# Optimization experiments

Measured on AMD Instinct MI355X. Metric: run time of the kernel, lower is better.

Reference implementation:

```python
import jax, jax.numpy as jnp
import numpy as np

N_NODES = 100000
N_EDGES = 3200000
D = 64
NUM_RELS = 20
HID_ATTR = 32
OUT_ATTR = 10


def setup_inputs() -> dict:
    key = jax.random.key(0)
    ks = jax.random.split(key, 10)
    h = jax.random.normal(ks[0], (N_NODES, D), dtype=jnp.float32)
    src = jax.random.randint(ks[1], (N_EDGES,), 0, N_NODES)
    dst = jax.random.randint(ks[2], (N_EDGES,), 0, N_NODES)
    etype = jax.random.randint(ks[3], (N_EDGES,), 0, NUM_RELS)
    # RGCN relation weights (num_bases == num_rels, so no basis decomposition)
    s1 = (2.0 / (D + D)) ** 0.5 * (2.0 ** 0.5)  # xavier w/ relu gain, approx
    W1 = jax.random.normal(ks[4], (NUM_RELS, D, D), dtype=jnp.float32) * s1
    W2 = jax.random.normal(ks[5], (NUM_RELS, D, D), dtype=jnp.float32) * s1
    # Attributor MLP params (torch Linear: y = x @ W.T + b; stored here as [in,out])
    A1_w = jax.random.normal(ks[6], (D, HID_ATTR), dtype=jnp.float32) * (1.0 / D ** 0.5)
    A1_b = jnp.zeros((HID_ATTR,), dtype=jnp.float32)
    A2_w = jax.random.normal(ks[7], (HID_ATTR, OUT_ATTR), dtype=jnp.float32) * (1.0 / HID_ATTR ** 0.5)
    A2_b = jnp.zeros((OUT_ATTR,), dtype=jnp.float32)
    return {"h": h, "src": src, "dst": dst, "etype": etype,
            "W1": W1, "W2": W2, "A1_w": A1_w, "A1_b": A1_b,
            "A2_w": A2_w, "A2_b": A2_b}


def _rgcn_layer(h, W, src, dst, etype, activation):
    # Transform all nodes by every relation once (avoids [E,d,d] weight gather),
    # then gather the relation-specific transformed source feature per edge.
    n = h.shape[0]
    t = jnp.einsum('nd,rdo->rno', h, W)          # [R, N, d_out]
    msg = t[etype, src]                           # [E, d_out] irregular gather
    agg = jax.ops.segment_sum(msg, dst, num_segments=n)  # scatter-sum to nodes
    return activation(agg) if activation is not None else agg


def reference(h, src, dst, etype, W1, W2, A1_w, A1_b, A2_w, A2_b):
    # hidden RGCN layer (relu), output RGCN layer (no activation, no bias)
    h1 = _rgcn_layer(h, W1, src, dst, etype, jax.nn.relu)
    h2 = _rgcn_layer(h1, W2, src, dst, etype, None)
    # mean_nodes over the single graph -> [1, D]; Attributor MLP (dropout in eval = identity)
    g = jnp.mean(h2, axis=0, keepdims=True)
    a = jax.nn.relu(g @ A1_w + A1_b)
    a = jax.nn.sigmoid(a @ A2_w + A2_b)
    return (h2, a)
```

## Files before the change

kernel.cpp:

```cpp
#include <hip/hip_runtime.h>
#include <hip/hip_bf16.h>
#include <math.h>
#include <stdint.h>

#define N_NODES 100000
#define N_EDGES 3200000
#define D 64
#define NUM_RELS 20
#define HID_ATTR 32
#define OUT_ATTR 10
#define PADR 72

#define BUCKET_DSTS 256
#define NB 391
#define PA_THREADS 512
#define PA_EPT 16
#define PA_CHUNK (PA_THREADS * PA_EPT)
#define PA_GRID 391
#define PB_BINS (BUCKET_DSTS * NUM_RELS)
#define REL_HALF 10

typedef __attribute__((ext_vector_type(8))) short bf16x8;
typedef __attribute__((ext_vector_type(4))) float f32x4;

static __device__ __forceinline__ unsigned short f2bf(float x) {
    unsigned u = __builtin_bit_cast(unsigned, x);
    unsigned r = (u + 0x7FFFu + ((u >> 16) & 1u)) >> 16;
    return (unsigned short)r;
}
static __device__ __forceinline__ float bf2f(unsigned short b) {
    return __builtin_bit_cast(float, (unsigned)b << 16);
}
static __device__ __forceinline__ float bf2f_lo(unsigned u) {
    return __builtin_bit_cast(float, u << 16);
}
static __device__ __forceinline__ float bf2f_hi(unsigned u) {
    return __builtin_bit_cast(float, u & 0xFFFF0000u);
}
static __device__ __forceinline__ unsigned cvt_pk_bf16(float lo, float hi) {
    unsigned r;
    asm("v_cvt_pk_bf16_f32 %0, %1, %2" : "=v"(r) : "v"(lo), "v"(hi));
    return r;
}


__global__ void hist_bucket_kernel(const int* __restrict__ dst, int* __restrict__ hist) {
    __shared__ int h[NB];
    for (int i = threadIdx.x; i < NB; i += PA_THREADS) h[i] = 0;
    __syncthreads();
    int base = blockIdx.x * PA_CHUNK;
#pragma unroll
    for (int k = 0; k < PA_EPT; ++k) {
        int e = base + k * PA_THREADS + threadIdx.x;
        if (e < N_EDGES) atomicAdd(&h[dst[e] >> 8], 1);
    }
    __syncthreads();
    for (int i = threadIdx.x; i < NB; i += PA_THREADS)
        if (h[i]) atomicAdd(&hist[i], h[i]);
}

__global__ void scan_bucket_kernel(const int* __restrict__ hist, int* __restrict__ bbase,
                                   int* __restrict__ bcur, int* __restrict__ off_node) {
    __shared__ int s[512];
    int t = threadIdx.x;
    int v = (t < NB) ? hist[t] : 0;
    s[t] = v;
    __syncthreads();
    for (int d2 = 1; d2 < 512; d2 <<= 1) {
        int x = (t >= d2) ? s[t - d2] : 0;
        __syncthreads();
        s[t] += x;
        __syncthreads();
    }
    if (t < NB) {
        int b = s[t] - v;
        bbase[t] = b;
        bcur[t] = b;
    }
    if (t == 0) {
        bbase[NB] = N_EDGES;
        off_node[N_NODES] = N_EDGES;
    }
}

__global__ __launch_bounds__(PA_THREADS) void passA_kernel(
    const int* __restrict__ src, const int* __restrict__ dst,
    const int* __restrict__ etype, int* __restrict__ bcur,
    unsigned* __restrict__ tmp) {
    __shared__ int h[NB];
    __shared__ int gb[NB];
    __shared__ int c[NB];
    for (int i = threadIdx.x; i < NB; i += PA_THREADS) h[i] = 0;
    __syncthreads();
    int base = blockIdx.x * PA_CHUNK;
    int d[PA_EPT];
#pragma unroll
    for (int k = 0; k < PA_EPT; ++k) {
        int e = base + k * PA_THREADS + threadIdx.x;
        d[k] = (e < N_EDGES) ? dst[e] : -1;
        if (d[k] >= 0) atomicAdd(&h[d[k] >> 8], 1);
    }
    __syncthreads();
    for (int i = threadIdx.x; i < NB; i += PA_THREADS) {
        int n = h[i];
        gb[i] = n ? atomicAdd(&bcur[i], n) : 0;
        c[i] = 0;
    }
    __syncthreads();
#pragma unroll
    for (int k = 0; k < PA_EPT; ++k) {
        int e = base + k * PA_THREADS + threadIdx.x;
        if (d[k] >= 0) {
            int b = d[k] >> 8;
            int sv = src[e], r = etype[e];
            int pos = gb[b] + atomicAdd(&c[b], 1);
            tmp[pos] = ((unsigned)(d[k] & 255) << 22) | ((unsigned)sv << 5) | (unsigned)r;
        }
    }
}

__global__ __launch_bounds__(512) void passB_kernel(
    const unsigned* __restrict__ tmp, const int* __restrict__ bbase,
    int* __restrict__ edgedata, int* __restrict__ off_node,
    int* __restrict__ off_half) {
    __shared__ int binpos[PB_BINS];
    __shared__ int ssum[512];
    int t = threadIdx.x;
    int b = blockIdx.x;
    int beg = bbase[b], end = bbase[b + 1];
    for (int i = t; i < PB_BINS; i += 512) binpos[i] = 0;
    __syncthreads();
    for (int i = beg + t; i < end; i += 512) {
        unsigned v = tmp[i];
        int key = (int)(v >> 22) * NUM_RELS + (int)(v & 31u);
        atomicAdd(&binpos[key], 1);
    }
    __syncthreads();
    int loc[10];
    int sum = 0;
#pragma unroll
    for (int j = 0; j < 10; ++j) {
        loc[j] = sum;
        sum += binpos[t * 10 + j];
    }
    ssum[t] = sum;
    __syncthreads();
    for (int d2 = 1; d2 < 512; d2 <<= 1) {
        int x = (t >= d2) ? ssum[t - d2] : 0;
        __syncthreads();
        ssum[t] += x;
        __syncthreads();
    }
    int tbase = beg + ((t > 0) ? ssum[t - 1] : 0);
#pragma unroll
    for (int j = 0; j < 10; ++j) binpos[t * 10 + j] = tbase + loc[j];
    __syncthreads();
    for (int dl = t; dl < BUCKET_DSTS; dl += 512) {
        off_node[b * BUCKET_DSTS + dl] = binpos[dl * NUM_RELS];
        off_half[b * BUCKET_DSTS + dl] = binpos[dl * NUM_RELS + REL_HALF];
    }
    __syncthreads();
    for (int i = beg + t; i < end; i += 512) {
        unsigned v = tmp[i];
        int key = (int)(v >> 22) * NUM_RELS + (int)(v & 31u);
        int pos = atomicAdd(&binpos[key], 1);
        edgedata[pos] = (int)(((v >> 5) & 0x1FFFFu) | ((v & 31u) << 17));
    }
}


__global__ void f2b_kernel(const float* __restrict__ in, unsigned short* __restrict__ out,
                           int n4) {
    int i = blockIdx.x * 256 + threadIdx.x;
    if (i >= n4) return;
    float4 v = ((const float4*)in)[i];
    ushort4 o;
    o.x = f2bf(v.x); o.y = f2bf(v.y); o.z = f2bf(v.z); o.w = f2bf(v.w);
    ((ushort4*)out)[i] = o;
}

__global__ void wconv_kernel(const float* __restrict__ W, unsigned short* __restrict__ Wb) {
    int r = blockIdx.x;
    for (int i = threadIdx.x; i < D * D; i += 256) {
        int d2 = i >> 6, o = i & 63;
        Wb[(size_t)r * (D * D) + o * D + d2] = f2bf(W[(size_t)r * (D * D) + d2 * D + o]);
    }
}

__global__ __launch_bounds__(512, 6) void fused_layer(
    const unsigned short* __restrict__ xb, const unsigned short* __restrict__ Wb,
    const int* __restrict__ edgedata, const int* __restrict__ off_node,
    const int* __restrict__ off_half,
    unsigned short* __restrict__ xbout, float* __restrict__ h2out, int mode) {
    __shared__ __align__(16) unsigned short A[NUM_RELS * 16 * PADR];
    int wave = threadIdx.x >> 6, lane = threadIdx.x & 63;
    int grp = lane >> 4, l4 = lane & 15;
    int gidx = wave * 4 + grp;
    int m = gidx & 15;
    int h = gidx >> 4;
    int colb = l4 * 4;

    for (int i = threadIdx.x; i < NUM_RELS * 16 * PADR / 8; i += 512)
        ((int4*)A)[i] = (int4){0, 0, 0, 0};
    __syncthreads();

    int n0 = blockIdx.x * 16;
    int node = n0 + m;
    int beg = h ? off_half[node] : off_node[node];
    int end = h ? off_node[node + 1] : off_half[node];
    int cnt = end - beg;
    int nb = (cnt + 7) >> 3;
    int nbmax = max(nb, __shfl_xor(nb, 16));
    nbmax = max(nbmax, __shfl_xor(nbmax, 32));
    int endm1 = end - 1;

    float a0 = 0.f, a1 = 0.f, a2 = 0.f, a3 = 0.f;
    int qcur = -1;
    unsigned short* Am = A + (unsigned)m * PADR + (unsigned)colb;

    auto rowload = [&](int ewv) -> uint2 {
        return *(const uint2*)(xb + (((unsigned)(ewv & 0x1FFFF)) << 6)
                               + (unsigned)colb);
    };
    auto proc = [&](int (&ewc)[8], uint2 (&xv)[8], int valid) {
#pragma unroll
        for (int j = 0; j < 8; ++j) {
            int q = ewc[j] >> 17;
            bool real = j < valid;
            unsigned mx = real ? xv[j].x : 0u;
            unsigned my = real ? xv[j].y : 0u;
            bool keep = (q == qcur);
            a0 = (keep ? a0 : 0.f) + bf2f_lo(mx);
            a1 = (keep ? a1 : 0.f) + bf2f_hi(mx);
            a2 = (keep ? a2 : 0.f) + bf2f_lo(my);
            a3 = (keep ? a3 : 0.f) + bf2f_hi(my);
            uint2 o;
            o.x = cvt_pk_bf16(a0, a1);
            o.y = cvt_pk_bf16(a2, a3);
            *(uint2*)(Am + (unsigned)q * (16 * PADR)) = o;
            qcur = q;
        }
    };

    int ewA[8], ewB[8];
    uint2 xvA[8], xvB[8];
    if (nb > 0) {
#pragma unroll
        for (int j = 0; j < 8; ++j) ewA[j] = edgedata[min(beg + j, endm1)];
    }
    if (nb > 1) {
#pragma unroll
        for (int j = 0; j < 8; ++j) ewB[j] = edgedata[min(beg + 8 + j, endm1)];
    }
    if (nb > 0) {
#pragma unroll
        for (int j = 0; j < 8; ++j) xvA[j] = rowload(ewA[j]);
    }

    for (int g = 0; g < nbmax;) {
        {
            bool act = g < nb;
            if (act) {
                int ewc[8];
#pragma unroll
                for (int j = 0; j < 8; ++j) ewc[j] = ewA[j];
                int nbase = beg + (g + 2) * 8;
                if (g + 2 < nb) {
#pragma unroll
                    for (int j = 0; j < 8; ++j)
                        ewA[j] = edgedata[min(nbase + j, endm1)];
                }
                if (g + 1 < nb) {
#pragma unroll
                    for (int j = 0; j < 8; ++j) xvB[j] = rowload(ewB[j]);
                }
                proc(ewc, xvA, cnt - g * 8);
            }
        }
        ++g;
        if (g >= nbmax) break;
        {
            bool act = g < nb;
            if (act) {
                int ewc[8];
#pragma unroll
                for (int j = 0; j < 8; ++j) ewc[j] = ewB[j];
                int nbase = beg + (g + 2) * 8;
                if (g + 2 < nb) {
#pragma unroll
                    for (int j = 0; j < 8; ++j)
                        ewB[j] = edgedata[min(nbase + j, endm1)];
                }
                if (g + 1 < nb) {
#pragma unroll
                    for (int j = 0; j < 8; ++j) xvA[j] = rowload(ewA[j]);
                }
                proc(ewc, xvB, cnt - g * 8);
            }
        }
        ++g;
    }
    __syncthreads();

    if (wave < 4) {
        int lrow = lane & 15, lhi = lane >> 4;
        f32x4 C = {0.f, 0.f, 0.f, 0.f};
        for (int q = 0; q < NUM_RELS; ++q) {
            const unsigned short* Arow = &A[(q * 16 + lrow) * PADR + lhi * 8];
            bf16x8 aa0 = *(const bf16x8*)(Arow);
            bf16x8 aa1 = *(const bf16x8*)(Arow + 32);
            const unsigned short* wrow = Wb + ((size_t)q << 12)
                                         + (size_t)(wave * 16 + lrow) * D + lhi * 8;
            bf16x8 b0 = *(const bf16x8*)(wrow);
            bf16x8 b1 = *(const bf16x8*)(wrow + 32);
            C = __builtin_amdgcn_mfma_f32_16x16x32_bf16(aa0, b0, C, 0, 0, 0);
            C = __builtin_amdgcn_mfma_f32_16x16x32_bf16(aa1, b1, C, 0, 0, 0);
        }
#pragma unroll
        for (int reg = 0; reg < 4; ++reg) {
            int onode = n0 + lhi * 4 + reg;
            int col = wave * 16 + lrow;
            if (mode == 1)
                xbout[(size_t)onode * D + col] = f2bf(fmaxf(C[reg], 0.f));
            else
                h2out[(size_t)onode * D + col] = C[reg];
        }
    }
}


__global__ void colsum_kernel(const float* __restrict__ h2,
                              float* __restrict__ g, int n) {
    __shared__ float s[256];
    int tid = threadIdx.x;
    int col = tid & 63;
    int rowgrp = (blockIdx.x * blockDim.x + tid) >> 6;
    int nrowgrp = (gridDim.x * blockDim.x) >> 6;
    float acc = 0.0f;
    for (int row = rowgrp; row < n; row += nrowgrp)
        acc += h2[(size_t)row * D + col];
    s[tid] = acc;
    __syncthreads();
    if (tid < 64) {
        acc = s[tid] + s[tid + 64] + s[tid + 128] + s[tid + 192];
        atomicAdd(&g[col], acc);
    }
}

__global__ void mlp_kernel(const float* __restrict__ g,
                           const float* __restrict__ A1w,
                           const float* __restrict__ A1b,
                           const float* __restrict__ A2w,
                           const float* __restrict__ A2b,
                           float* __restrict__ out, float invN) {
    __shared__ float a1[HID_ATTR];
    int t = threadIdx.x;
    if (t < HID_ATTR) {
        float acc = A1b[t];
#pragma unroll
        for (int d2 = 0; d2 < D; ++d2)
            acc = fmaf(g[d2] * invN, A1w[d2 * HID_ATTR + t], acc);
        a1[t] = fmaxf(acc, 0.0f);
    }
    __syncthreads();
    if (t < OUT_ATTR) {
        float acc = A2b[t];
#pragma unroll
        for (int j = 0; j < HID_ATTR; ++j)
            acc = fmaf(a1[j], A2w[j * OUT_ATTR + t], acc);
        out[t] = 1.0f / (1.0f + expf(-acc));
    }
}


extern "C" void kernel_launch(void* const* d_in, const int* in_sizes, int n_in,
                              void* d_out, int out_size, void* d_ws, size_t ws_size,
                              hipStream_t stream) {
    const float* h   = (const float*)d_in[0];
    const int* src   = (const int*)d_in[1];
    const int* dst   = (const int*)d_in[2];
    const int* etype = (const int*)d_in[3];
    const float* W1  = (const float*)d_in[4];
    const float* W2  = (const float*)d_in[5];
    const float* A1w = (const float*)d_in[6];
    const float* A1b = (const float*)d_in[7];
    const float* A2w = (const float*)d_in[8];
    const float* A2b = (const float*)d_in[9];

    float* out_h2 = (float*)d_out;
    float* out_a  = out_h2 + (size_t)N_NODES * D;

    int* base       = (int*)d_ws;
    float* gsum     = (float*)base;
    int* hist_b     = base + 64;
    int* bbase      = base + 456;
    int* bcur       = base + 848;
    int* off_node   = base + 1240;
    int* off_half   = base + 101592;
    unsigned* tmp   = (unsigned*)(base + 201944);
    int* edgedata   = base + 3401944;
    unsigned short* xb  = (unsigned short*)(base + 6601944);
    unsigned short* xb2 = (unsigned short*)(base + 9801944);
    unsigned short* w1b = (unsigned short*)(base + 13001944);
    unsigned short* w2b = (unsigned short*)(base + 13042904);

    hipMemsetAsync(hist_b, 0, NB * sizeof(int), stream);
    hipMemsetAsync(gsum, 0, 64 * sizeof(float), stream);

    hist_bucket_kernel<<<PA_GRID, PA_THREADS, 0, stream>>>(dst, hist_b);
    scan_bucket_kernel<<<1, 512, 0, stream>>>(hist_b, bbase, bcur, off_node);
    passA_kernel<<<PA_GRID, PA_THREADS, 0, stream>>>(src, dst, etype, bcur, tmp);
    passB_kernel<<<NB, 512, 0, stream>>>(tmp, bbase, edgedata, off_node, off_half);

    wconv_kernel<<<NUM_RELS, 256, 0, stream>>>(W1, w1b);
    wconv_kernel<<<NUM_RELS, 256, 0, stream>>>(W2, w2b);
    f2b_kernel<<<(N_NODES * D / 4 + 255) / 256, 256, 0, stream>>>(h, xb, N_NODES * D / 4);

    fused_layer<<<N_NODES / 16, 512, 0, stream>>>(xb, w1b, edgedata, off_node,
                                                  off_half, xb2, nullptr, 1);
    fused_layer<<<N_NODES / 16, 512, 0, stream>>>(xb2, w2b, edgedata, off_node,
                                                  off_half, nullptr, out_h2, 2);

    colsum_kernel<<<512, 256, 0, stream>>>(out_h2, gsum, N_NODES);
    mlp_kernel<<<1, 64, 0, stream>>>(gsum, A1w, A1b, A2w, A2b,
                                     out_a, 1.0f / (float)N_NODES);
}
```

Baseline: 601.8 us.

## Balance per-group edge work via sorted quarter-node segments paired longest-with-shortest

After: 576.0 us. -4.3%, faster.

```diff
diff --git a/kernel.cpp b/kernel.cpp
--- a/kernel.cpp
+++ b/kernel.cpp
@@ -10,6 +10,7 @@
 #define HID_ATTR 32
 #define OUT_ATTR 10
 #define PADR 72
+#define NFB (N_NODES / 16)
 
 #define BUCKET_DSTS 256
 #define NB 391
@@ -18,7 +19,6 @@
 #define PA_CHUNK (PA_THREADS * PA_EPT)
 #define PA_GRID 391
 #define PB_BINS (BUCKET_DSTS * NUM_RELS)
-#define REL_HALF 10
 
 typedef __attribute__((ext_vector_type(8))) short bf16x8;
 typedef __attribute__((ext_vector_type(4))) float f32x4;
@@ -60,7 +60,7 @@
 }
 
 __global__ void scan_bucket_kernel(const int* __restrict__ hist, int* __restrict__ bbase,
-                                   int* __restrict__ bcur, int* __restrict__ off_node) {
+                                   int* __restrict__ bcur, int* __restrict__ sched_off) {
     __shared__ int s[512];
     int t = threadIdx.x;
     int v = (t < NB) ? hist[t] : 0;
@@ -79,7 +79,7 @@
     }
     if (t == 0) {
         bbase[NB] = N_EDGES;
-        off_node[N_NODES] = N_EDGES;
+        sched_off[NFB * 32] = N_EDGES;
     }
 }
 
@@ -121,10 +121,14 @@
 
 __global__ __launch_bounds__(512) void passB_kernel(
     const unsigned* __restrict__ tmp, const int* __restrict__ bbase,
-    int* __restrict__ edgedata, int* __restrict__ off_node,
-    int* __restrict__ off_half) {
+    unsigned* __restrict__ edgedata, int* __restrict__ sched_off) {
     __shared__ int binpos[PB_BINS];
+    __shared__ int blen[PB_BINS];
+    __shared__ unsigned sk[16 * 64];
+    __shared__ int swo[16 * 64];
+    __shared__ int gs[512];
     __shared__ int ssum[512];
+    __shared__ int fbb[16];
     int t = threadIdx.x;
     int b = blockIdx.x;
     int beg = bbase[b], end = bbase[b + 1];
@@ -135,6 +139,8 @@
         int key = (int)(v >> 22) * NUM_RELS + (int)(v & 31u);
         atomicAdd(&binpos[key], 1);
     }
+    __syncthreads();
+    for (int i = t; i < PB_BINS; i += 512) blen[i] = binpos[i];
     __syncthreads();
     int loc[10];
     int sum = 0;
@@ -155,16 +161,69 @@
 #pragma unroll
     for (int j = 0; j < 10; ++j) binpos[t * 10 + j] = tbase + loc[j];
     __syncthreads();
-    for (int dl = t; dl < BUCKET_DSTS; dl += 512) {
-        off_node[b * BUCKET_DSTS + dl] = binpos[dl * NUM_RELS];
-        off_half[b * BUCKET_DSTS + dl] = binpos[dl * NUM_RELS + REL_HALF];
+    if (t < 16) fbb[t] = binpos[t * 320];
+    __syncthreads();
+    for (int w = t; w < 1024; w += 512) {
+        int fb = w >> 6, wloc = w & 63;
+        int nl = wloc >> 2, qt = wloc & 3;
+        int b0 = (fb * 16 + nl) * NUM_RELS + qt * 5;
+        int len = blen[b0] + blen[b0 + 1] + blen[b0 + 2] + blen[b0 + 3] + blen[b0 + 4];
+        sk[fb * 64 + wloc] = ((unsigned)len << 8) | (unsigned)wloc;
+    }
+    {
+        int fb = t >> 5, k = t & 31;
+        unsigned* s = &sk[fb * 64];
+        for (int size = 2; size <= 64; size <<= 1) {
+            for (int stride = size >> 1; stride > 0; stride >>= 1) {
+                __syncthreads();
+                int i1 = ((k & ~(stride - 1)) << 1) | (k & (stride - 1));
+                int i2 = i1 | stride;
+                unsigned x = s[i1], y = s[i2];
+                bool descb = (i1 & size) == 0;
+                if (descb ? (x < y) : (x > y)) { s[i1] = y; s[i2] = x; }
+            }
+        }
+    }
+    __syncthreads();
+    {
+        int fb = t >> 5, k = t & 31;
+        unsigned kA = sk[fb * 64 + k], kB = sk[fb * 64 + 63 - k];
+        int lenA = (int)(kA >> 8), widA = (int)(kA & 63u);
+        int lenB = (int)(kB >> 8), widB = (int)(kB & 63u);
+        int tot = lenA + lenB;
+        gs[t] = tot;
+        __syncthreads();
+        for (int d2 = 1; d2 < 32; d2 <<= 1) {
+            int x = (k >= d2) ? gs[t - d2] : 0;
+            __syncthreads();
+            gs[t] += x;
+            __syncthreads();
+        }
+        int gbase = gs[t] - tot;
+        swo[fb * 64 + widA] = gbase;
+        swo[fb * 64 + widB] = gbase + lenA;
+        int gfb = b * 16 + fb;
+        if (gfb < NFB) sched_off[gfb * 32 + k] = fbb[fb] + gbase;
+    }
+    __syncthreads();
+    for (int i = t; i < PB_BINS; i += 512) {
+        int node = i / 20, rel = i - node * 20;
+        int fb = node >> 4, nl = node & 15;
+        int qt = rel / 5, rr = rel - qt * 5;
+        int wid = nl * 4 + qt;
+        int base = fbb[fb] + swo[fb * 64 + wid];
+        int b0 = node * 20 + qt * 5;
+        for (int r = 0; r < rr; ++r) base += blen[b0 + r];
+        binpos[i] = base;
     }
     __syncthreads();
     for (int i = beg + t; i < end; i += 512) {
         unsigned v = tmp[i];
-        int key = (int)(v >> 22) * NUM_RELS + (int)(v & 31u);
+        int dl = (int)(v >> 22), rel = (int)(v & 31u);
+        int ro = rel * (16 * PADR) + (dl & 15) * PADR;
+        int key = dl * NUM_RELS + rel;
         int pos = atomicAdd(&binpos[key], 1);
-        edgedata[pos] = (int)(((v >> 5) & 0x1FFFFu) | ((v & 31u) << 17));
+        edgedata[pos] = ((v >> 5) & 0x1FFFFu) | ((unsigned)ro << 17);
     }
 }
 
@@ -189,25 +248,20 @@
 
 __global__ __launch_bounds__(512, 6) void fused_layer(
     const unsigned short* __restrict__ xb, const unsigned short* __restrict__ Wb,
-    const int* __restrict__ edgedata, const int* __restrict__ off_node,
-    const int* __restrict__ off_half,
+    const unsigned* __restrict__ edgedata, const int* __restrict__ sched_off,
     unsigned short* __restrict__ xbout, float* __restrict__ h2out, int mode) {
     __shared__ __align__(16) unsigned short A[NUM_RELS * 16 * PADR];
     int wave = threadIdx.x >> 6, lane = threadIdx.x & 63;
     int grp = lane >> 4, l4 = lane & 15;
     int gidx = wave * 4 + grp;
-    int m = gidx & 15;
-    int h = gidx >> 4;
     int colb = l4 * 4;
 
     for (int i = threadIdx.x; i < NUM_RELS * 16 * PADR / 8; i += 512)
         ((int4*)A)[i] = (int4){0, 0, 0, 0};
     __syncthreads();
 
-    int n0 = blockIdx.x * 16;
-    int node = n0 + m;
-    int beg = h ? off_half[node] : off_node[node];
-    int end = h ? off_node[node + 1] : off_half[node];
+    int beg = sched_off[blockIdx.x * 32 + gidx];
+    int end = sched_off[blockIdx.x * 32 + gidx + 1];
     int cnt = end - beg;
     int nb = (cnt + 7) >> 3;
     int nbmax = max(nb, __shfl_xor(nb, 16));
@@ -215,21 +269,20 @@
     int endm1 = end - 1;
 
     float a0 = 0.f, a1 = 0.f, a2 = 0.f, a3 = 0.f;
-    int qcur = -1;
-    unsigned short* Am = A + (unsigned)m * PADR + (unsigned)colb;
-
-    auto rowload = [&](int ewv) -> uint2 {
-        return *(const uint2*)(xb + (((unsigned)(ewv & 0x1FFFF)) << 6)
-                               + (unsigned)colb);
+    unsigned roprev = 0xFFFFFFFFu;
+    unsigned short* Ac = A + (unsigned)colb;
+
+    auto rowload = [&](unsigned ewv) -> uint2 {
+        return *(const uint2*)(xb + ((ewv & 0x1FFFFu) << 6) + (unsigned)colb);
     };
-    auto proc = [&](int (&ewc)[8], uint2 (&xv)[8], int valid) {
+    auto proc = [&](unsigned (&ewc)[8], uint2 (&xv)[8], int valid) {
 #pragma unroll
         for (int j = 0; j < 8; ++j) {
-            int q = ewc[j] >> 17;
+            unsigned ro = ewc[j] >> 17;
             bool real = j < valid;
             unsigned mx = real ? xv[j].x : 0u;
             unsigned my = real ? xv[j].y : 0u;
-            bool keep = (q == qcur);
+            bool keep = (ro == roprev);
             a0 = (keep ? a0 : 0.f) + bf2f_lo(mx);
             a1 = (keep ? a1 : 0.f) + bf2f_hi(mx);
             a2 = (keep ? a2 : 0.f) + bf2f_lo(my);
@@ -237,12 +290,12 @@
             uint2 o;
             o.x = cvt_pk_bf16(a0, a1);
             o.y = cvt_pk_bf16(a2, a3);
-            *(uint2*)(Am + (unsigned)q * (16 * PADR)) = o;
-            qcur = q;
+            *(uint2*)(Ac + ro) = o;
+            roprev = ro;
         }
     };
 
-    int ewA[8], ewB[8];
+    unsigned ewA[8], ewB[8];
     uint2 xvA[8], xvB[8];
     if (nb > 0) {
 #pragma unroll
@@ -261,7 +314,7 @@
         {
             bool act = g < nb;
             if (act) {
-                int ewc[8];
+                unsigned ewc[8];
 #pragma unroll
                 for (int j = 0; j < 8; ++j) ewc[j] = ewA[j];
                 int nbase = beg + (g + 2) * 8;
@@ -282,7 +335,7 @@
         {
             bool act = g < nb;
             if (act) {
-                int ewc[8];
+                unsigned ewc[8];
 #pragma unroll
                 for (int j = 0; j < 8; ++j) ewc[j] = ewB[j];
                 int nbase = beg + (g + 2) * 8;
@@ -318,7 +371,7 @@
         }
 #pragma unroll
         for (int reg = 0; reg < 4; ++reg) {
-            int onode = n0 + lhi * 4 + reg;
+            int onode = blockIdx.x * 16 + lhi * 4 + reg;
             int col = wave * 16 + lrow;
             if (mode == 1)
                 xbout[(size_t)onode * D + col] = f2bf(fmaxf(C[reg], 0.f));
@@ -393,33 +446,32 @@
     int* base       = (int*)d_ws;
     float* gsum     = (float*)base;
     int* hist_b     = base + 64;
-    int* bbase      = base + 456;
-    int* bcur       = base + 848;
-    int* off_node   = base + 1240;
-    int* off_half   = base + 101592;
-    unsigned* tmp   = (unsigned*)(base + 201944);
-    int* edgedata   = base + 3401944;
-    unsigned short* xb  = (unsigned short*)(base + 6601944);
-    unsigned short* xb2 = (unsigned short*)(base + 9801944);
-    unsigned short* w1b = (unsigned short*)(base + 13001944);
-    unsigned short* w2b = (unsigned short*)(base + 13042904);
+    int* bbase      = base + 512;
+    int* bcur       = base + 960;
+    int* sched_off  = base + 1408;
+    unsigned* tmp   = (unsigned*)(base + 201472);
+    unsigned* edgedata = (unsigned*)(base + 3401472);
+    unsigned short* xb  = (unsigned short*)(base + 6601472);
+    unsigned short* xb2 = (unsigned short*)(base + 9801472);
+    unsigned short* w1b = (unsigned short*)(base + 13001472);
+    unsigned short* w2b = (unsigned short*)(base + 13042432);
 
     hipMemsetAsync(hist_b, 0, NB * sizeof(int), stream);
     hipMemsetAsync(gsum, 0, 64 * sizeof(float), stream);
 
     hist_bucket_kernel<<<PA_GRID, PA_THREADS, 0, stream>>>(dst, hist_b);
-    scan_bucket_kernel<<<1, 512, 0, stream>>>(hist_b, bbase, bcur, off_node);
+    scan_bucket_kernel<<<1, 512, 0, stream>>>(hist_b, bbase, bcur, sched_off);
     passA_kernel<<<PA_GRID, PA_THREADS, 0, stream>>>(src, dst, etype, bcur, tmp);
-    passB_kernel<<<NB, 512, 0, stream>>>(tmp, bbase, edgedata, off_node, off_half);
+    passB_kernel<<<NB, 512, 0, stream>>>(tmp, bbase, edgedata, sched_off);
 
     wconv_kernel<<<NUM_RELS, 256, 0, stream>>>(W1, w1b);
     wconv_kernel<<<NUM_RELS, 256, 0, stream>>>(W2, w2b);
     f2b_kernel<<<(N_NODES * D / 4 + 255) / 256, 256, 0, stream>>>(h, xb, N_NODES * D / 4);
 
-    fused_layer<<<N_NODES / 16, 512, 0, stream>>>(xb, w1b, edgedata, off_node,
-                                                  off_half, xb2, nullptr, 1);
-    fused_layer<<<N_NODES / 16, 512, 0, stream>>>(xb2, w2b, edgedata, off_node,
-                                                  off_half, nullptr, out_h2, 2);
+    fused_layer<<<NFB, 512, 0, stream>>>(xb, w1b, edgedata, sched_off,
+                                         xb2, nullptr, 1);
+    fused_layer<<<NFB, 512, 0, stream>>>(xb2, w2b, edgedata, sched_off,
+                                         nullptr, out_h2, 2);
 
     colsum_kernel<<<512, 256, 0, stream>>>(out_h2, gsum, N_NODES);
     mlp_kernel<<<1, 64, 0, stream>>>(gsum, A1w, A1b, A2w, A2b,
```
